# Optimization experiments

Measured on AMD Instinct MI355X. Metric: run time of the kernel, lower is better.

Reference implementation:

```python
import jax, jax.numpy as jnp
import numpy as np

NUM_NODES = 200000
NUM_GRAPHS = 1024
D_FEAT = 512


def setup_inputs() -> dict:
    key = jax.random.key(0)
    k_x, k_j = jax.random.split(key)
    inputs = jax.random.normal(k_x, (NUM_NODES, D_FEAT), dtype=jnp.float32)
    # Contiguous, strictly-increasing segment start offsets with idx[0] == 0.
    # Base offsets split nodes ~evenly; jitter in [0, step) keeps strict monotonicity.
    step = NUM_NODES // NUM_GRAPHS  # 195
    base = (jnp.arange(NUM_GRAPHS, dtype=jnp.int32) * NUM_NODES) // NUM_GRAPHS
    jitter = jax.random.randint(k_j, (NUM_GRAPHS,), 0, step, dtype=jnp.int32)
    idx = base + jitter
    idx = idx.at[0].set(0)
    return {"inputs": inputs, "idx": idx, "num_nodes": NUM_NODES, "num_graphs": NUM_GRAPHS}


def reference(inputs, idx, num_nodes, num_graphs):
    # Original: dense [num_graphs, num_nodes] pooling matrix with row i holding
    # 1/(idx[i+1]-idx[i]) over columns idx[i]:idx[i+1], then matmul + relu.
    # Equivalent math: per-contiguous-segment mean of node features, then relu.
    node_ids = jnp.arange(num_nodes, dtype=jnp.int32)
    # segment id of node n: largest i with idx[i] <= n (idx[0]=0 -> seg >= 0)
    seg = jnp.searchsorted(idx, node_ids, side="right") - 1  # [num_nodes]
    sums = jax.ops.segment_sum(inputs, seg, num_segments=num_graphs)  # [G, D]
    idx_aug = jnp.append(idx, jnp.int32(num_nodes))
    counts = (idx_aug[1:] - idx_aug[:-1]).astype(inputs.dtype)  # [G]
    out = sums / counts[:, None]
    return jax.nn.relu(out)
```

## Files before the change

kernel.cpp:

```cpp
#include <hip/hip_runtime.h>


#define D_FEAT 512
#define NCOL4 (D_FEAT / 4)

__global__ __launch_bounds__(256) void zero_out_kernel(float4* __restrict__ out,
                                                       int n4) {
  int i = blockIdx.x * blockDim.x + threadIdx.x;
  if (i < n4) out[i] = make_float4(0.f, 0.f, 0.f, 0.f);
}

__global__ __launch_bounds__(512) void seg_accum_kernel(
    const float4* __restrict__ in,
    const int* __restrict__ idx,
    float* __restrict__ out,
    int num_nodes, int num_graphs, int rows_per_blk) {
  const int r0 = blockIdx.x * rows_per_blk;
  if (r0 >= num_nodes) return;
  const int r1 = min(r0 + rows_per_blk, num_nodes);

  const int col = threadIdx.x & (NCOL4 - 1);
  const int grp = threadIdx.x >> 7;

  int lo = 0, hi = num_graphs - 1;
  while (lo < hi) {
    int mid = (lo + hi + 1) >> 1;
    if (idx[mid] <= r0) lo = mid;
    else hi = mid - 1;
  }
  int s = lo;
  int row = r0;

  __shared__ float4 part[3][NCOL4];

  while (row < r1) {
    const int seg_end = (s + 1 < num_graphs) ? idx[s + 1] : num_nodes;
    const int e = min(seg_end, r1);

    float4 acc = make_float4(0.f, 0.f, 0.f, 0.f);
    for (int r = row + grp; r < e; r += 4) {
      float4 v = in[(size_t)r * NCOL4 + col];
      acc.x += v.x;
      acc.y += v.y;
      acc.z += v.z;
      acc.w += v.w;
    }

    if (grp > 0) part[grp - 1][col] = acc;
    __syncthreads();
    if (grp == 0) {
#pragma unroll
      for (int g = 0; g < 3; ++g) {
        float4 p = part[g][col];
        acc.x += p.x;
        acc.y += p.y;
        acc.z += p.z;
        acc.w += p.w;
      }
      float* o = out + (size_t)s * D_FEAT + col * 4;
      atomicAdd(o + 0, acc.x);
      atomicAdd(o + 1, acc.y);
      atomicAdd(o + 2, acc.z);
      atomicAdd(o + 3, acc.w);
    }
    __syncthreads();

    row = e;
    ++s;
  }
}

__global__ __launch_bounds__(256) void finalize_kernel(
    float* __restrict__ out, const int* __restrict__ idx, int num_nodes,
    int num_graphs) {
  int i = blockIdx.x * blockDim.x + threadIdx.x;
  int total4 = num_graphs * NCOL4;
  if (i >= total4) return;
  int g = i >> 7;
  int start = idx[g];
  int end = (g + 1 < num_graphs) ? idx[g + 1] : num_nodes;
  float sInv = 1.0f / (float)(end - start);
  float4* o4 = (float4*)out;
  float4 v = o4[i];
  v.x = fmaxf(v.x * sInv, 0.f);
  v.y = fmaxf(v.y * sInv, 0.f);
  v.z = fmaxf(v.z * sInv, 0.f);
  v.w = fmaxf(v.w * sInv, 0.f);
  o4[i] = v;
}

extern "C" void kernel_launch(void* const* d_in, const int* in_sizes, int n_in,
                              void* d_out, int out_size, void* d_ws,
                              size_t ws_size, hipStream_t stream) {
  const float4* in = (const float4*)d_in[0];
  const int* idx = (const int*)d_in[1];
  float* out = (float*)d_out;

  const int num_nodes = in_sizes[0] / D_FEAT;
  const int num_graphs = in_sizes[1];

  const int out4 = num_graphs * NCOL4;
  zero_out_kernel<<<dim3((out4 + 255) / 256), dim3(256), 0, stream>>>(
      (float4*)out, out4);

  const int nblocks = 1024;
  const int rows_per_blk = (num_nodes + nblocks - 1) / nblocks;
  seg_accum_kernel<<<dim3(nblocks), dim3(512), 0, stream>>>(
      in, idx, out, num_nodes, num_graphs, rows_per_blk);

  finalize_kernel<<<dim3((out4 + 255) / 256), dim3(256), 0, stream>>>(
      out, idx, num_nodes, num_graphs);
}
```

Before: 88.82 us.

## Split segment rows across waves with flat contiguous unrolled float4 loads

Reworks the segment accumulation so each of the eight wavefronts takes a contiguous row range of the segment and streams it as a flat float4 array, with four independent loads in flight per iteration and two accumulators split by column half. Partial sums from all eight waves are reduced through shared memory before the atomic adds. The aim is more memory-level parallelism and better streaming access than the old four-group strided row loop. It adds a larger shared buffer and an eight-way reduction, and guards the finalize step against empty segments.

```diff
diff --git a/kernel.cpp b/kernel.cpp
--- a/kernel.cpp
+++ b/kernel.cpp
@@ -19,8 +19,12 @@
   if (r0 >= num_nodes) return;
   const int r1 = min(r0 + rows_per_blk, num_nodes);
 
-  const int col = threadIdx.x & (NCOL4 - 1);
-  const int grp = threadIdx.x >> 7;
+  const int lane = threadIdx.x & 63;
+  const int w = threadIdx.x >> 6;
+  const int col = threadIdx.x & 127;
+  const int g = threadIdx.x >> 7;
+
+  __shared__ float4 part[8][NCOL4];
 
   int lo = 0, hi = num_graphs - 1;
   while (lo < hi) {
@@ -31,37 +35,54 @@
   int s = lo;
   int row = r0;
 
-  __shared__ float4 part[3][NCOL4];
-
   while (row < r1) {
     const int seg_end = (s + 1 < num_graphs) ? idx[s + 1] : num_nodes;
     const int e = min(seg_end, r1);
+    const int n = e - row;
 
-    float4 acc = make_float4(0.f, 0.f, 0.f, 0.f);
-    for (int r = row + grp; r < e; r += 4) {
-      float4 v = in[(size_t)r * NCOL4 + col];
-      acc.x += v.x;
-      acc.y += v.y;
-      acc.z += v.z;
-      acc.w += v.w;
+    const int ws = row + (n * w) / 8;
+    const int we = row + (n * (w + 1)) / 8;
+
+    float4 accA = make_float4(0.f, 0.f, 0.f, 0.f);
+    float4 accB = make_float4(0.f, 0.f, 0.f, 0.f);
+
+    int j = ws * NCOL4 + lane;
+    const int jend = we * NCOL4;
+    for (; j + 192 < jend; j += 256) {
+      float4 v0 = in[j];
+      float4 v1 = in[j + 64];
+      float4 v2 = in[j + 128];
+      float4 v3 = in[j + 192];
+      accA.x += v0.x; accA.y += v0.y; accA.z += v0.z; accA.w += v0.w;
+      accB.x += v1.x; accB.y += v1.y; accB.z += v1.z; accB.w += v1.w;
+      accA.x += v2.x; accA.y += v2.y; accA.z += v2.z; accA.w += v2.w;
+      accB.x += v3.x; accB.y += v3.y; accB.z += v3.z; accB.w += v3.w;
+    }
+    for (; j < jend; j += 64) {
+      float4 v = in[j];
+      if ((((j - lane) >> 6) & 1) == 0) {
+        accA.x += v.x; accA.y += v.y; accA.z += v.z; accA.w += v.w;
+      } else {
+        accB.x += v.x; accB.y += v.y; accB.z += v.z; accB.w += v.w;
+      }
     }
 
-    if (grp > 0) part[grp - 1][col] = acc;
+    part[w][lane] = accA;
+    part[w][lane + 64] = accB;
     __syncthreads();
-    if (grp == 0) {
+
+    if (g == 0) {
+      float4 a = part[0][col];
 #pragma unroll
-      for (int g = 0; g < 3; ++g) {
-        float4 p = part[g][col];
-        acc.x += p.x;
-        acc.y += p.y;
-        acc.z += p.z;
-        acc.w += p.w;
+      for (int ww = 1; ww < 8; ++ww) {
+        float4 p = part[ww][col];
+        a.x += p.x; a.y += p.y; a.z += p.z; a.w += p.w;
       }
       float* o = out + (size_t)s * D_FEAT + col * 4;
-      atomicAdd(o + 0, acc.x);
-      atomicAdd(o + 1, acc.y);
-      atomicAdd(o + 2, acc.z);
-      atomicAdd(o + 3, acc.w);
+      atomicAdd(o + 0, a.x);
+      atomicAdd(o + 1, a.y);
+      atomicAdd(o + 2, a.z);
+      atomicAdd(o + 3, a.w);
     }
     __syncthreads();
 
@@ -76,10 +97,11 @@
   int i = blockIdx.x * blockDim.x + threadIdx.x;
   int total4 = num_graphs * NCOL4;
   if (i >= total4) return;
-  int g = i >> 7;
-  int start = idx[g];
-  int end = (g + 1 < num_graphs) ? idx[g + 1] : num_nodes;
-  float sInv = 1.0f / (float)(end - start);
+  int gph = i >> 7;
+  int start = idx[gph];
+  int end = (gph + 1 < num_graphs) ? idx[gph + 1] : num_nodes;
+  int cnt = end - start;
+  float sInv = (cnt > 0) ? 1.0f / (float)cnt : 0.0f;
   float4* o4 = (float4*)out;
   float4 v = o4[i];
   v.x = fmaxf(v.x * sInv, 0.f);
```

After: 88.79 us. No clear change (-0.0%).

## Fuse zero, accumulate and finalize into one cooperative kernel with grid sync

Applied to the files above, without the earlier changes.

Replaces the three launches (zeroing, atomic segment accumulation, finalize) with a single cooperative kernel. Each block writes up to four per-segment partial sums to a workspace, then after a grid-wide sync each block reduces the partials for one graph and applies the mean and relu. This removes two kernel launches and the global float atomics. The cost is a grid barrier, a cooperative launch that needs all 1024 blocks resident at once, and workspace round trips. It also assumes no block spans more than four segments.

```diff
diff --git a/kernel.cpp b/kernel.cpp
--- a/kernel.cpp
+++ b/kernel.cpp
@@ -1,92 +1,94 @@
 #include <hip/hip_runtime.h>
+#include <hip/hip_cooperative_groups.h>
+
+namespace cg = cooperative_groups;
 
 
 #define D_FEAT 512
 #define NCOL4 (D_FEAT / 4)
+#define MAX_SUB 4
 
-__global__ __launch_bounds__(256) void zero_out_kernel(float4* __restrict__ out,
-                                                       int n4) {
-  int i = blockIdx.x * blockDim.x + threadIdx.x;
-  if (i < n4) out[i] = make_float4(0.f, 0.f, 0.f, 0.f);
-}
-
-__global__ __launch_bounds__(512) void seg_accum_kernel(
+__global__ __launch_bounds__(512) void fused_pool_kernel(
     const float4* __restrict__ in,
     const int* __restrict__ idx,
     float* __restrict__ out,
+    float* __restrict__ ws,
     int num_nodes, int num_graphs, int rows_per_blk) {
-  const int r0 = blockIdx.x * rows_per_blk;
-  if (r0 >= num_nodes) return;
-  const int r1 = min(r0 + rows_per_blk, num_nodes);
-
+  const int b = blockIdx.x;
   const int col = threadIdx.x & (NCOL4 - 1);
   const int grp = threadIdx.x >> 7;
 
-  int lo = 0, hi = num_graphs - 1;
-  while (lo < hi) {
-    int mid = (lo + hi + 1) >> 1;
-    if (idx[mid] <= r0) lo = mid;
-    else hi = mid - 1;
-  }
-  int s = lo;
-  int row = r0;
-
   __shared__ float4 part[3][NCOL4];
 
-  while (row < r1) {
-    const int seg_end = (s + 1 < num_graphs) ? idx[s + 1] : num_nodes;
-    const int e = min(seg_end, r1);
+  const int r0 = b * rows_per_blk;
+  if (r0 < num_nodes) {
+    const int r1 = min(r0 + rows_per_blk, num_nodes);
 
-    float4 acc = make_float4(0.f, 0.f, 0.f, 0.f);
-    for (int r = row + grp; r < e; r += 4) {
-      float4 v = in[(size_t)r * NCOL4 + col];
-      acc.x += v.x;
-      acc.y += v.y;
-      acc.z += v.z;
-      acc.w += v.w;
+    int lo = 0, hi = num_graphs - 1;
+    while (lo < hi) {
+      int mid = (lo + hi + 1) >> 1;
+      if (idx[mid] <= r0) lo = mid;
+      else hi = mid - 1;
     }
+    int s = lo;
+    int row = r0;
+    int k = 0;
 
-    if (grp > 0) part[grp - 1][col] = acc;
-    __syncthreads();
-    if (grp == 0) {
+    while (row < r1 && k < MAX_SUB) {
+      const int seg_end = (s + 1 < num_graphs) ? idx[s + 1] : num_nodes;
+      const int e = min(seg_end, r1);
+
+      float4 acc = make_float4(0.f, 0.f, 0.f, 0.f);
+      for (int r = row + grp; r < e; r += 4) {
+        float4 v = in[(size_t)r * NCOL4 + col];
+        acc.x += v.x; acc.y += v.y; acc.z += v.z; acc.w += v.w;
+      }
+
+      if (grp > 0) part[grp - 1][col] = acc;
+      __syncthreads();
+      if (grp == 0) {
 #pragma unroll
-      for (int g = 0; g < 3; ++g) {
-        float4 p = part[g][col];
-        acc.x += p.x;
-        acc.y += p.y;
-        acc.z += p.z;
-        acc.w += p.w;
+        for (int g = 0; g < 3; ++g) {
+          float4 p = part[g][col];
+          acc.x += p.x; acc.y += p.y; acc.z += p.z; acc.w += p.w;
+        }
+        ((float4*)ws)[((size_t)b * MAX_SUB + k) * NCOL4 + col] = acc;
       }
-      float* o = out + (size_t)s * D_FEAT + col * 4;
-      atomicAdd(o + 0, acc.x);
-      atomicAdd(o + 1, acc.y);
-      atomicAdd(o + 2, acc.z);
-      atomicAdd(o + 3, acc.w);
+      __syncthreads();
+
+      row = e;
+      ++s;
+      ++k;
     }
-    __syncthreads();
+  }
 
-    row = e;
-    ++s;
+  __threadfence();
+  cg::this_grid().sync();
+
+  const int s = b;
+  if (s < num_graphs) {
+    const int t = threadIdx.x;
+    const int start = idx[s];
+    const int end = (s + 1 < num_graphs) ? idx[s + 1] : num_nodes;
+    const int b0 = start / rows_per_blk;
+    const int b1 = (end - 1) / rows_per_blk;
+
+    float sum = 0.f;
+    for (int bb = b0; bb <= b1; ++bb) {
+      const int rr = bb * rows_per_blk;
+      int lo = 0, hi = num_graphs - 1;
+      while (lo < hi) {
+        int mid = (lo + hi + 1) >> 1;
+        if (idx[mid] <= rr) lo = mid;
+        else hi = mid - 1;
+      }
+      const int local = s - lo;
+      if (local >= 0 && local < MAX_SUB)
+        sum += ws[((size_t)bb * MAX_SUB + local) * D_FEAT + t];
+    }
+    const float inv = 1.0f / (float)(end - start);
+    out[(size_t)s * D_FEAT + t] = fmaxf(sum * inv, 0.f);
   }
-}
-
-__global__ __launch_bounds__(256) void finalize_kernel(
-    float* __restrict__ out, const int* __restrict__ idx, int num_nodes,
-    int num_graphs) {
-  int i = blockIdx.x * blockDim.x + threadIdx.x;
-  int total4 = num_graphs * NCOL4;
-  if (i >= total4) return;
-  int g = i >> 7;
-  int start = idx[g];
-  int end = (g + 1 < num_graphs) ? idx[g + 1] : num_nodes;
-  float sInv = 1.0f / (float)(end - start);
-  float4* o4 = (float4*)out;
-  float4 v = o4[i];
-  v.x = fmaxf(v.x * sInv, 0.f);
-  v.y = fmaxf(v.y * sInv, 0.f);
-  v.z = fmaxf(v.z * sInv, 0.f);
-  v.w = fmaxf(v.w * sInv, 0.f);
-  o4[i] = v;
 }
 
 extern "C" void kernel_launch(void* const* d_in, const int* in_sizes, int n_in,
@@ -95,19 +97,16 @@
   const float4* in = (const float4*)d_in[0];
   const int* idx = (const int*)d_in[1];
   float* out = (float*)d_out;
+  float* ws = (float*)d_ws;
 
-  const int num_nodes = in_sizes[0] / D_FEAT;
-  const int num_graphs = in_sizes[1];
+  int num_nodes = in_sizes[0] / D_FEAT;
+  int num_graphs = in_sizes[1];
 
-  const int out4 = num_graphs * NCOL4;
-  zero_out_kernel<<<dim3((out4 + 255) / 256), dim3(256), 0, stream>>>(
-      (float4*)out, out4);
+  int nblocks = num_graphs;
+  int rows_per_blk = (num_nodes + nblocks - 1) / nblocks;
 
-  const int nblocks = 1024;
-  const int rows_per_blk = (num_nodes + nblocks - 1) / nblocks;
-  seg_accum_kernel<<<dim3(nblocks), dim3(512), 0, stream>>>(
-      in, idx, out, num_nodes, num_graphs, rows_per_blk);
-
-  finalize_kernel<<<dim3((out4 + 255) / 256), dim3(256), 0, stream>>>(
-      out, idx, num_nodes, num_graphs);
+  void* args[] = {(void*)&in, (void*)&idx, (void*)&out, (void*)&ws,
+                  (void*)&num_nodes, (void*)&num_graphs, (void*)&rows_per_blk};
+  hipLaunchCooperativeKernel((const void*)fused_pool_kernel, dim3(nblocks),
+                             dim3(512), args, 0, stream);
 }
```

Result: slower. 337.1 us (+279.5%).
